# Kernel tuning notes

Measured on AMD Instinct MI355X. Metric: run time of the kernel, lower is better.

## Reference

```python
import jax, jax.numpy as jnp
import numpy as np

EPS = 0.1
MAX_ITER = 100
THRESH = 0.1


def setup_inputs() -> dict:
    key = jax.random.key(0)
    k1, k2, k3, k4 = jax.random.split(key, 4)
    N, P1, P2, D = 4, 1024, 1024, 16
    x = jax.random.normal(k1, (N, P1, D), dtype=jnp.float32)
    y = jax.random.normal(k2, (N, P2, D), dtype=jnp.float32)
    wx = jax.random.uniform(k3, (N, P1), dtype=jnp.float32)
    wy = jax.random.uniform(k4, (N, P2), dtype=jnp.float32)
    # normalize to probability weights (typical usage for empirical measures)
    wx = wx / jnp.sum(wx, axis=-1, keepdims=True)
    wy = wy / jnp.sum(wy, axis=-1, keepdims=True)
    return {"x": x, "y": y, "wx": wx, "wy": wy}


def _cost_matrix(x, y):
    # |x_i - y_j|^1 summed over feature dim -> [N, P1, P2]
    return jnp.sum(jnp.abs(x[:, :, None, :] - y[:, None, :, :]), axis=-1)


def reference(x, y, wx, wy):
    C = _cost_matrix(x, y)                     # [N, P1, P2]
    mu, nu = wx, wy                            # [N, P1], [N, P2]
    log_mu = jnp.log(mu + 1e-8)
    log_nu = jnp.log(nu + 1e-8)

    def M(u, v):
        # (-C_ij + u_i + v_j) / eps
        return (-C + u[:, :, None] + v[:, None, :]) / EPS

    def step(carry, _):
        u, v, done = carry
        u_new = EPS * (log_mu - jax.nn.logsumexp(M(u, v), axis=-1)) + u
        v_new = EPS * (log_nu - jax.nn.logsumexp(M(u_new, v), axis=-2)) + v
        err = jnp.mean(jnp.sum(jnp.abs(u_new - u), axis=-1))
        # emulate torch's early break: freeze u,v once converged
        u_out = jnp.where(done, u, u_new)
        v_out = jnp.where(done, v, v_new)
        done = done | (err < THRESH)
        return (u_out, v_out, done), None

    u0 = jnp.zeros_like(mu)
    v0 = jnp.zeros_like(nu)
    (u, v, _), _ = jax.lax.scan(step, (u0, v0, jnp.array(False)), None, length=MAX_ITER)

    pi = jnp.exp(M(u, v))                      # transport plan [N, P1, P2]
    cost = jnp.sum(pi * C, axis=(-2, -1))      # [N]  (reduction='none')
    return cost, pi, C
```

## Files before the change

### kernel.cpp

```cpp
#include <hip/hip_runtime.h>

static constexpr int   NB      = 4;
static constexpr int   PP      = 1024;
static constexpr int   DD      = 16;
static constexpr float EPSV    = 0.1f;
static constexpr float KE      = 14.42695041f;
static constexpr float KL      = 0.0693147181f;
static constexpr int   MAXIT   = 100;
static constexpr float THRESHV = 0.1f;

static constexpr int NBLK = 256;
static constexpr int NTHR = 512;
static constexpr unsigned DONEG = 1000000u;

static constexpr int    ERR_F_OFF     = 4352;
static constexpr size_t WS_ZERO_BYTES = 4352 * 4;
static constexpr size_t ERR_BYTES     = 512 * 4;

static constexpr int VSNAP_OFF = 131072;

__device__ __forceinline__ float fexp2(float v) { return __builtin_amdgcn_exp2f(v); }
__device__ __forceinline__ float flog2(float v) { return __builtin_amdgcn_logf(v); }

__device__ __forceinline__ float aload(const float* p) {
    return __hip_atomic_load(p, __ATOMIC_RELAXED, __HIP_MEMORY_SCOPE_AGENT);
}
__device__ __forceinline__ void astore(float* p, float v) {
    __hip_atomic_store(p, v, __ATOMIC_RELAXED, __HIP_MEMORY_SCOPE_AGENT);
}
__device__ __forceinline__ unsigned aloadu(const unsigned* p) {
    return __hip_atomic_load(p, __ATOMIC_RELAXED, __HIP_MEMORY_SCOPE_AGENT);
}
__device__ __forceinline__ void astoreu(unsigned* p, unsigned v) {
    __hip_atomic_store(p, v, __ATOMIC_RELAXED, __HIP_MEMORY_SCOPE_AGENT);
}
__device__ __forceinline__ float2 aload2(const float* p) {
    unsigned long long v = __hip_atomic_load((const unsigned long long*)p,
                                             __ATOMIC_RELAXED, __HIP_MEMORY_SCOPE_AGENT);
    union { unsigned long long u; float f[2]; } c; c.u = v;
    return make_float2(c.f[0], c.f[1]);
}
__device__ __forceinline__ void astore2(float* p, float a, float b) {
    union { unsigned long long u; float f[2]; } c; c.f[0] = a; c.f[1] = b;
    __hip_atomic_store((unsigned long long*)p, c.u,
                       __ATOMIC_RELAXED, __HIP_MEMORY_SCOPE_AGENT);
}

__device__ __forceinline__ int pidx(int e) { return (e >> 4) * 17 + (e & 15); }

__device__ __forceinline__ void stage_poll(const unsigned* ws32, int n,
                                           const float* src, unsigned gen,
                                           float* sbuf2, int tid) {
    if (tid < 64) {
        const unsigned* sp = ws32 + (n * 64 + tid) * 16;
        const float* cp = src + tid * 16;
        float2 d0, d1, d2, d3, d4, d5, d6, d7;
        bool got = false;
        for (;;) {
            if (!got && aloadu(sp) >= gen) {
                d0 = aload2(cp + 0);  d1 = aload2(cp + 2);
                d2 = aload2(cp + 4);  d3 = aload2(cp + 6);
                d4 = aload2(cp + 8);  d5 = aload2(cp + 10);
                d6 = aload2(cp + 12); d7 = aload2(cp + 14);
                got = true;
            }
            if (__ballot(got) == ~0ull) break;
            __builtin_amdgcn_s_sleep(1);
        }
        float* dst = sbuf2 + tid * 17;
        dst[0]  = d0.x; dst[1]  = d0.y; dst[2]  = d1.x; dst[3]  = d1.y;
        dst[4]  = d2.x; dst[5]  = d2.y; dst[6]  = d3.x; dst[7]  = d3.y;
        dst[8]  = d4.x; dst[9]  = d4.y; dst[10] = d5.x; dst[11] = d5.y;
        dst[12] = d6.x; dst[13] = d6.y; dst[14] = d7.x; dst[15] = d7.y;
    }
}

__device__ __forceinline__ void gbar_group(unsigned* ws32, int n, int g, unsigned gen) {
    __syncthreads();
    if (threadIdx.x < 64) {
        if (threadIdx.x == 0) astoreu(ws32 + (n * 64 + g) * 16, gen);
        const unsigned* sp = ws32 + (n * 64 + threadIdx.x) * 16;
        while (__ballot(aloadu(sp) >= gen) != ~0ull)
            __builtin_amdgcn_s_sleep(1);
    }
    __syncthreads();
}

__global__ __launch_bounds__(NTHR, 2)
void sinkhorn_kernel(const float* __restrict__ x, const float* __restrict__ y,
                     const float* __restrict__ wx, const float* __restrict__ wy,
                     float* __restrict__ out, float* __restrict__ ws)
{
    __shared__ float rt[16 * PP];
    __shared__ float sbuf2[1088];
    __shared__ float cred[8];
    __shared__ int   Ts;
    __shared__ int   s_ef;

    unsigned* ws32  = (unsigned*)ws;
    unsigned* Tslot = ws32 + 4096;
    unsigned* exitf = ws32 + 4104;
    float*    ews   = ws + ERR_F_OFF;

    float* out_cost = out;
    float* out_pi   = out + NB;
    float* out_C    = out + NB + (size_t)NB * PP * PP;

    const int b   = blockIdx.x;
    const int n   = b >> 6;
    const int g   = b & 63;
    const int i0  = g * 16;
    const int w   = threadIdx.x >> 6;
    const int l   = threadIdx.x & 63;
    const int tid = threadIdx.x;

    float* sc = out_C + (size_t)n * PP * PP;

    if (tid == 0) s_ef = 0;

    float4 xr[2][4];
    #pragma unroll
    for (int rr = 0; rr < 2; ++rr) {
        const float4* xp = (const float4*)(x + ((size_t)n * PP + (i0 + 2 * w + rr)) * DD);
        #pragma unroll
        for (int q = 0; q < 4; ++q) xr[rr][q] = xp[q];
    }
    #pragma unroll 4
    for (int k = 0; k < 16; ++k) {
        int j = l + 64 * k;
        const float4* yp = (const float4*)(y + ((size_t)n * PP + j) * DD);
        float4 y0 = yp[0], y1 = yp[1], y2 = yp[2], y3 = yp[3];
        #pragma unroll
        for (int rr = 0; rr < 2; ++rr) {
            float c = fabsf(xr[rr][0].x - y0.x) + fabsf(xr[rr][0].y - y0.y)
                    + fabsf(xr[rr][0].z - y0.z) + fabsf(xr[rr][0].w - y0.w)
                    + fabsf(xr[rr][1].x - y1.x) + fabsf(xr[rr][1].y - y1.y)
                    + fabsf(xr[rr][1].z - y1.z) + fabsf(xr[rr][1].w - y1.w)
                    + fabsf(xr[rr][2].x - y2.x) + fabsf(xr[rr][2].y - y2.y)
                    + fabsf(xr[rr][2].z - y2.z) + fabsf(xr[rr][2].w - y2.w)
                    + fabsf(xr[rr][3].x - y3.x) + fabsf(xr[rr][3].y - y3.y)
                    + fabsf(xr[rr][3].z - y3.z) + fabsf(xr[rr][3].w - y3.w);
            rt[(2 * w + rr) * PP + j] = c;
        }
    }

    float4 yc[2][4];
    #pragma unroll
    for (int c = 0; c < 2; ++c) {
        const float4* yp = (const float4*)(y + ((size_t)n * PP + (i0 + 2 * w + c)) * DD);
        #pragma unroll
        for (int q = 0; q < 4; ++q) yc[c][q] = yp[q];
    }
    float2 c2[16];
    #pragma unroll 4
    for (int k = 0; k < 16; ++k) {
        const float4* xp = (const float4*)(x + ((size_t)n * PP + (l + 64 * k)) * DD);
        float4 x0 = xp[0], x1 = xp[1], x2 = xp[2], x3 = xp[3];
        float cc[2];
        #pragma unroll
        for (int c = 0; c < 2; ++c) {
            cc[c] = fabsf(x0.x - yc[c][0].x) + fabsf(x0.y - yc[c][0].y)
                  + fabsf(x0.z - yc[c][0].z) + fabsf(x0.w - yc[c][0].w)
                  + fabsf(x1.x - yc[c][1].x) + fabsf(x1.y - yc[c][1].y)
                  + fabsf(x1.z - yc[c][1].z) + fabsf(x1.w - yc[c][1].w)
                  + fabsf(x2.x - yc[c][2].x) + fabsf(x2.y - yc[c][2].y)
                  + fabsf(x2.z - yc[c][2].z) + fabsf(x2.w - yc[c][2].w)
                  + fabsf(x3.x - yc[c][3].x) + fabsf(x3.y - yc[c][3].y)
                  + fabsf(x3.z - yc[c][3].z) + fabsf(x3.w - yc[c][3].w);
        }
        c2[k] = make_float2(cc[0], cc[1]);
    }

    float lmu[2], lnu[2];
    #pragma unroll
    for (int rr = 0; rr < 2; ++rr) {
        lmu[rr] = __logf(wx[n * PP + i0 + 2 * w + rr] + 1e-8f);
        lnu[rr] = __logf(wy[n * PP + i0 + 2 * w + rr] + 1e-8f);
    }

    float uprev0 = 0.f, uprev1 = 0.f;

    int last_t = 0;

    #pragma unroll 1
    for (int t = 0; t < MAXIT; ++t) {
        if (t >= 2 && s_ef != 0 && t >= s_ef + 1) break;
        last_t = t;

        if (t == 0) {
            sbuf2[pidx(2 * tid)] = 0.f; sbuf2[pidx(2 * tid + 1)] = 0.f;
        } else {
            stage_poll(ws32, n, sc + VSNAP_OFF + (size_t)(t - 1) * PP,
                       (unsigned)(2 * t), sbuf2, tid);
        }
        __syncthreads();

        {
            float4 tt[2][4];
            float m0 = -3.4e38f, m1 = -3.4e38f;
            #pragma unroll
            for (int k = 0; k < 4; ++k) {
                int j = 256 * k + 4 * l;
                float v0 = sbuf2[pidx(j)],     v1 = sbuf2[pidx(j + 1)];
                float v2 = sbuf2[pidx(j + 2)], v3 = sbuf2[pidx(j + 3)];
                float4 ca = *(const float4*)&rt[(2 * w) * PP + j];
                float4 cb = *(const float4*)&rt[(2 * w + 1) * PP + j];
                tt[0][k] = make_float4(v0 - ca.x, v1 - ca.y, v2 - ca.z, v3 - ca.w);
                tt[1][k] = make_float4(v0 - cb.x, v1 - cb.y, v2 - cb.z, v3 - cb.w);
                m0 = fmaxf(m0, fmaxf(fmaxf(tt[0][k].x, tt[0][k].y), fmaxf(tt[0][k].z, tt[0][k].w)));
                m1 = fmaxf(m1, fmaxf(fmaxf(tt[1][k].x, tt[1][k].y), fmaxf(tt[1][k].z, tt[1][k].w)));
            }
            #pragma unroll
            for (int off = 32; off >= 1; off >>= 1) {
                m0 = fmaxf(m0, __shfl_xor(m0, off));
                m1 = fmaxf(m1, __shfl_xor(m1, off));
            }
            float s0 = 0.f, s1 = 0.f;
            #pragma unroll
            for (int k = 0; k < 4; ++k) {
                s0 += fexp2((tt[0][k].x - m0) * KE) + fexp2((tt[0][k].y - m0) * KE)
                    + fexp2((tt[0][k].z - m0) * KE) + fexp2((tt[0][k].w - m0) * KE);
                s1 += fexp2((tt[1][k].x - m1) * KE) + fexp2((tt[1][k].y - m1) * KE)
                    + fexp2((tt[1][k].z - m1) * KE) + fexp2((tt[1][k].w - m1) * KE);
            }
            #pragma unroll
            for (int off = 32; off >= 1; off >>= 1) {
                s0 += __shfl_xor(s0, off);
                s1 += __shfl_xor(s1, off);
            }
            float un0 = EPSV * lmu[0] - (m0 + KL * flog2(s0));
            float un1 = EPSV * lmu[1] - (m1 + KL * flog2(s1));
            if (l == 0) astore2(sc + (size_t)t * PP + i0 + 2 * w, un0, un1);
        }
        __syncthreads();
        if (tid == 0) astoreu(ws32 + (n * 64 + g) * 16, (unsigned)(2 * t + 1));

        stage_poll(ws32, n, sc + (size_t)t * PP, (unsigned)(2 * t + 1), sbuf2, tid);
        __syncthreads();

        {
            float up0 = sbuf2[pidx(2 * tid)], up1 = sbuf2[pidx(2 * tid + 1)];
            float we = fabsf(up0 - uprev0) + fabsf(up1 - uprev1);
            uprev0 = up0; uprev1 = up1;
            #pragma unroll
            for (int off = 32; off >= 1; off >>= 1) we += __shfl_xor(we, off);
            if (l == 0) cred[w] = we;
        }
        __syncthreads();

        {
            float tt0[16], tt1[16], m0 = -3.4e38f, m1 = -3.4e38f;
            #pragma unroll
            for (int k = 0; k < 16; ++k) {
                float uu = sbuf2[pidx(l + 64 * k)];
                tt0[k] = uu - c2[k].x;
                tt1[k] = uu - c2[k].y;
                m0 = fmaxf(m0, tt0[k]);
                m1 = fmaxf(m1, tt1[k]);
            }
            #pragma unroll
            for (int off = 32; off >= 1; off >>= 1) {
                m0 = fmaxf(m0, __shfl_xor(m0, off));
                m1 = fmaxf(m1, __shfl_xor(m1, off));
            }
            float s0 = 0.f, s1 = 0.f;
            #pragma unroll
            for (int k = 0; k < 16; ++k) {
                s0 += fexp2((tt0[k] - m0) * KE);
                s1 += fexp2((tt1[k] - m1) * KE);
            }
            #pragma unroll
            for (int off = 32; off >= 1; off >>= 1) {
                s0 += __shfl_xor(s0, off);
                s1 += __shfl_xor(s1, off);
            }
            float vn0 = EPSV * lnu[0] - (m0 + KL * flog2(s0));
            float vn1 = EPSV * lnu[1] - (m1 + KL * flog2(s1));
            if (l == 0)
                astore2(sc + VSNAP_OFF + (size_t)t * PP + i0 + 2 * w, vn0, vn1);
        }
        if (g == 0 && tid == 0) {
            float es = cred[0] + cred[1] + cred[2] + cred[3]
                     + cred[4] + cred[5] + cred[6] + cred[7];
            astore(ews + n * 128 + t, es);
        }

        __syncthreads();
        if (tid < 64) {
            if (tid == 0) astoreu(ws32 + (n * 64 + g) * 16, (unsigned)(2 * t + 2));
            if (g == 0) {
                float s1f = aload(ews + 0 * 128 + tid) + aload(ews + 1 * 128 + tid)
                          + aload(ews + 2 * 128 + tid) + aload(ews + 3 * 128 + tid);
                float s2f = aload(ews + 0 * 128 + 64 + tid) + aload(ews + 1 * 128 + 64 + tid)
                          + aload(ews + 2 * 128 + 64 + tid) + aload(ews + 3 * 128 + 64 + tid);
                unsigned long long bb = __ballot(s1f < THRESHV * (float)NB)
                                      | __ballot(s2f < THRESHV * (float)NB);
                if (bb != 0ull && tid == 0 && aloadu(exitf + n) == 0u)
                    astoreu(exitf + n, (unsigned)(t + 1));
            }
        }
        if (tid == 0) s_ef = (int)aloadu(exitf + n);
        __syncthreads();
    }

    {
        const unsigned need = (unsigned)(2 * last_t + 2);
        if (tid < 64) {
            const unsigned* sp = ws32 + (n * 64 + tid) * 16;
            while (__ballot(aloadu(sp) >= need) != ~0ull)
                __builtin_amdgcn_s_sleep(1);
        }
        __syncthreads();
    }

    if (g == 0 && tid == 0) astoreu(ws32 + (n * 64) * 16, DONEG);

    if (b == 0 && tid < 64) {
        for (;;) {
            bool ok = (tid >= 4) || (aloadu(ws32 + tid * 64 * 16) >= DONEG);
            if (__ballot(ok) == ~0ull) break;
            __builtin_amdgcn_s_sleep(2);
        }
        float s1f = aload(ews + 0 * 128 + tid) + aload(ews + 1 * 128 + tid)
                  + aload(ews + 2 * 128 + tid) + aload(ews + 3 * 128 + tid);
        float s2f = aload(ews + 0 * 128 + 64 + tid) + aload(ews + 1 * 128 + 64 + tid)
                  + aload(ews + 2 * 128 + 64 + tid) + aload(ews + 3 * 128 + 64 + tid);
        unsigned long long b1 = __ballot(s1f < THRESHV * (float)NB);
        unsigned long long b2 = __ballot(s2f < THRESHV * (float)NB);
        int T = b1 ? (__ffsll((long long)b1) - 1)
                   : (b2 ? 64 + (__ffsll((long long)b2) - 1) : MAXIT - 1);
        if (tid == 0) astoreu(Tslot, (unsigned)(T + 1));
    }
    if (tid == 0) {
        unsigned tv;
        while ((tv = aloadu(Tslot)) == 0u) __builtin_amdgcn_s_sleep(2);
        Ts = (int)tv - 1;
    }
    __syncthreads();
    const int T = Ts;

    float u_loc[2];
    {
        float2 up = aload2(sc + (size_t)T * PP + i0 + 2 * w);
        u_loc[0] = up.x; u_loc[1] = up.y;
        float2 vp = aload2(sc + VSNAP_OFF + (size_t)T * PP + 2 * tid);
        sbuf2[pidx(2 * tid)] = vp.x; sbuf2[pidx(2 * tid + 1)] = vp.y;
    }
    gbar_group(ws32, n, g, DONEG + 1u);

    float cacc = 0.f;
    #pragma unroll
    for (int rr = 0; rr < 2; ++rr) {
        int r = 2 * w + rr;
        int i = i0 + r;
        float un = u_loc[rr];
        #pragma unroll
        for (int k = 0; k < 4; ++k) {
            int j = 256 * k + 4 * l;
            float4 c4 = *(const float4*)&rt[r * PP + j];
            float v0 = sbuf2[pidx(j)],     v1 = sbuf2[pidx(j + 1)];
            float v2 = sbuf2[pidx(j + 2)], v3 = sbuf2[pidx(j + 3)];
            float4 p4;
            p4.x = fexp2((un + v0 - c4.x) * KE);
            p4.y = fexp2((un + v1 - c4.y) * KE);
            p4.z = fexp2((un + v2 - c4.z) * KE);
            p4.w = fexp2((un + v3 - c4.w) * KE);
            *(float4*)&out_pi[((size_t)n * PP + i) * PP + j] = p4;
            *(float4*)&out_C [((size_t)n * PP + i) * PP + j] = c4;
            cacc += p4.x * c4.x + p4.y * c4.y + p4.z * c4.z + p4.w * c4.w;
        }
    }
    #pragma unroll
    for (int off = 32; off >= 1; off >>= 1) cacc += __shfl_xor(cacc, off);
    if (l == 0) cred[w] = cacc;
    __syncthreads();
    if (tid == 0) {
        float s = 0.f;
        #pragma unroll
        for (int q = 0; q < 8; ++q) s += cred[q];
        atomicAdd(&out_cost[n], s);
    }
}

extern "C" void kernel_launch(void* const* d_in, const int* in_sizes, int n_in,
                              void* d_out, int out_size, void* d_ws, size_t ws_size,
                              hipStream_t stream) {
    const float* x  = (const float*)d_in[0];
    const float* y  = (const float*)d_in[1];
    const float* wx = (const float*)d_in[2];
    const float* wy = (const float*)d_in[3];
    float* out = (float*)d_out;
    float* ws  = (float*)d_ws;

    (void)hipMemsetAsync(d_ws, 0, WS_ZERO_BYTES, stream);
    (void)hipMemsetAsync((char*)d_ws + WS_ZERO_BYTES, 0x7f, ERR_BYTES, stream);
    (void)hipMemsetAsync(d_out, 0, NB * sizeof(float), stream);

    hipLaunchKernelGGL(sinkhorn_kernel, dim3(NBLK), dim3(NTHR), 0, stream,
                       x, y, wx, wy, out, ws);
}
```

Baseline: 797.1 us.

## Halve block count with 1024-thread blocks of 32 rows and XOR-swizzled LDS buffer

Each block now owns 32 rows with 1024 threads, so only 32 groups per batch take part in the per-iteration cross-block flag barrier instead of 64. The intent is to cut polling and synchronisation latency in each Sinkhorn half-step. The padded shared buffer (pidx) is replaced by an XOR-swizzled layout so u/v can be read as float4 without bank conflicts. The price is a larger LDS footprint (32 rows of cost per block) and more complex index mapping, with a risk of layout errors in the many hard-coded index paths.

```diff
diff --git a/kernel.cpp b/kernel.cpp
--- a/kernel.cpp
+++ b/kernel.cpp
@@ -9,8 +9,10 @@
 static constexpr int   MAXIT   = 100;
 static constexpr float THRESHV = 0.1f;
 
-static constexpr int NBLK = 256;
-static constexpr int NTHR = 512;
+static constexpr int NBLK = 128;
+static constexpr int NTHR = 1024;
+static constexpr int GPB  = 32;
+static constexpr int RPB  = 32;
 static constexpr unsigned DONEG = 1000000u;
 
 static constexpr int    ERR_F_OFF     = 4352;
@@ -46,54 +48,55 @@
                        __ATOMIC_RELAXED, __HIP_MEMORY_SCOPE_AGENT);
 }
 
-__device__ __forceinline__ int pidx(int e) { return (e >> 4) * 17 + (e & 15); }
 
 __device__ __forceinline__ void stage_poll(const unsigned* ws32, int n,
                                            const float* src, unsigned gen,
-                                           float* sbuf2, int tid) {
+                                           float* sbuf, int tid) {
     if (tid < 64) {
-        const unsigned* sp = ws32 + (n * 64 + tid) * 16;
-        const float* cp = src + tid * 16;
-        float2 d0, d1, d2, d3, d4, d5, d6, d7;
-        bool got = false;
+        const int t = tid & 31;
+        bool got = (tid >= 32);
+        const unsigned* sp = ws32 + (n * GPB + t) * 16;
+        const float* cp = src + t * RPB;
+        float2 d[16];
         for (;;) {
             if (!got && aloadu(sp) >= gen) {
-                d0 = aload2(cp + 0);  d1 = aload2(cp + 2);
-                d2 = aload2(cp + 4);  d3 = aload2(cp + 6);
-                d4 = aload2(cp + 8);  d5 = aload2(cp + 10);
-                d6 = aload2(cp + 12); d7 = aload2(cp + 14);
+                #pragma unroll
+                for (int q = 0; q < 16; ++q) d[q] = aload2(cp + 2 * q);
                 got = true;
             }
             if (__ballot(got) == ~0ull) break;
             __builtin_amdgcn_s_sleep(1);
         }
-        float* dst = sbuf2 + tid * 17;
-        dst[0]  = d0.x; dst[1]  = d0.y; dst[2]  = d1.x; dst[3]  = d1.y;
-        dst[4]  = d2.x; dst[5]  = d2.y; dst[6]  = d3.x; dst[7]  = d3.y;
-        dst[8]  = d4.x; dst[9]  = d4.y; dst[10] = d5.x; dst[11] = d5.y;
-        dst[12] = d6.x; dst[13] = d6.y; dst[14] = d7.x; dst[15] = d7.y;
+        if (tid < 32) {
+            #pragma unroll
+            for (int q = 0; q < 8; ++q) {
+                int p = (8 * t + q) ^ (t & 7);
+                *(float4*)&sbuf[4 * p] =
+                    make_float4(d[2 * q].x, d[2 * q].y, d[2 * q + 1].x, d[2 * q + 1].y);
+            }
+        }
     }
 }
 
 __device__ __forceinline__ void gbar_group(unsigned* ws32, int n, int g, unsigned gen) {
     __syncthreads();
     if (threadIdx.x < 64) {
-        if (threadIdx.x == 0) astoreu(ws32 + (n * 64 + g) * 16, gen);
-        const unsigned* sp = ws32 + (n * 64 + threadIdx.x) * 16;
-        while (__ballot(aloadu(sp) >= gen) != ~0ull)
+        if (threadIdx.x == 0) astoreu(ws32 + (n * GPB + g) * 16, gen);
+        const unsigned* sp = ws32 + (n * GPB + (threadIdx.x & 31)) * 16;
+        while (__ballot((threadIdx.x >= 32) || (aloadu(sp) >= gen)) != ~0ull)
             __builtin_amdgcn_s_sleep(1);
     }
     __syncthreads();
 }
 
-__global__ __launch_bounds__(NTHR, 2)
+__global__ __launch_bounds__(NTHR, 4)
 void sinkhorn_kernel(const float* __restrict__ x, const float* __restrict__ y,
                      const float* __restrict__ wx, const float* __restrict__ wy,
                      float* __restrict__ out, float* __restrict__ ws)
 {
-    __shared__ float rt[16 * PP];
-    __shared__ float sbuf2[1088];
-    __shared__ float cred[8];
+    __shared__ float rt[RPB * PP];
+    __shared__ float sbuf[PP];
+    __shared__ float cred[16];
     __shared__ int   Ts;
     __shared__ int   s_ef;
 
@@ -107,9 +110,9 @@
     float* out_C    = out + NB + (size_t)NB * PP * PP;
 
     const int b   = blockIdx.x;
-    const int n   = b >> 6;
-    const int g   = b & 63;
-    const int i0  = g * 16;
+    const int n   = b >> 5;
+    const int g   = b & (GPB - 1);
+    const int i0  = g * RPB;
     const int w   = threadIdx.x >> 6;
     const int l   = threadIdx.x & 63;
     const int tid = threadIdx.x;
@@ -117,6 +120,21 @@
     float* sc = out_C + (size_t)n * PP * PP;
 
     if (tid == 0) s_ef = 0;
+
+    const int lx = l ^ ((l >> 3) & 7);
+    int rv[16];
+    #pragma unroll
+    for (int k = 0; k < 16; ++k) {
+        int s = 16 * k + (l >> 2);
+        int p = s ^ ((2 * k + (l >> 5)) & 7);
+        rv[k] = 4 * p + (l & 3);
+    }
+    int ea;
+    {
+        int s = tid >> 1;
+        int p = s ^ ((tid >> 4) & 7);
+        ea = 4 * p + 2 * (tid & 1);
+    }
 
     float4 xr[2][4];
     #pragma unroll
@@ -188,10 +206,10 @@
         last_t = t;
 
         if (t == 0) {
-            sbuf2[pidx(2 * tid)] = 0.f; sbuf2[pidx(2 * tid + 1)] = 0.f;
+            if (tid < 512) { sbuf[ea] = 0.f; sbuf[ea + 1] = 0.f; }
         } else {
             stage_poll(ws32, n, sc + VSNAP_OFF + (size_t)(t - 1) * PP,
-                       (unsigned)(2 * t), sbuf2, tid);
+                       (unsigned)(2 * t), sbuf, tid);
         }
         __syncthreads();
 
@@ -201,12 +219,11 @@
             #pragma unroll
             for (int k = 0; k < 4; ++k) {
                 int j = 256 * k + 4 * l;
-                float v0 = sbuf2[pidx(j)],     v1 = sbuf2[pidx(j + 1)];
-                float v2 = sbuf2[pidx(j + 2)], v3 = sbuf2[pidx(j + 3)];
+                float4 v4 = *(const float4*)&sbuf[256 * k + 4 * lx];
                 float4 ca = *(const float4*)&rt[(2 * w) * PP + j];
                 float4 cb = *(const float4*)&rt[(2 * w + 1) * PP + j];
-                tt[0][k] = make_float4(v0 - ca.x, v1 - ca.y, v2 - ca.z, v3 - ca.w);
-                tt[1][k] = make_float4(v0 - cb.x, v1 - cb.y, v2 - cb.z, v3 - cb.w);
+                tt[0][k] = make_float4(v4.x - ca.x, v4.y - ca.y, v4.z - ca.z, v4.w - ca.w);
+                tt[1][k] = make_float4(v4.x - cb.x, v4.y - cb.y, v4.z - cb.z, v4.w - cb.w);
                 m0 = fmaxf(m0, fmaxf(fmaxf(tt[0][k].x, tt[0][k].y), fmaxf(tt[0][k].z, tt[0][k].w)));
                 m1 = fmaxf(m1, fmaxf(fmaxf(tt[1][k].x, tt[1][k].y), fmaxf(tt[1][k].z, tt[1][k].w)));
             }
@@ -233,13 +250,13 @@
             if (l == 0) astore2(sc + (size_t)t * PP + i0 + 2 * w, un0, un1);
         }
         __syncthreads();
-        if (tid == 0) astoreu(ws32 + (n * 64 + g) * 16, (unsigned)(2 * t + 1));
-
-        stage_poll(ws32, n, sc + (size_t)t * PP, (unsigned)(2 * t + 1), sbuf2, tid);
-        __syncthreads();
-
-        {
-            float up0 = sbuf2[pidx(2 * tid)], up1 = sbuf2[pidx(2 * tid + 1)];
+        if (tid == 0) astoreu(ws32 + (n * GPB + g) * 16, (unsigned)(2 * t + 1));
+
+        stage_poll(ws32, n, sc + (size_t)t * PP, (unsigned)(2 * t + 1), sbuf, tid);
+        __syncthreads();
+
+        if (tid < 512) {
+            float up0 = sbuf[ea], up1 = sbuf[ea + 1];
             float we = fabsf(up0 - uprev0) + fabsf(up1 - uprev1);
             uprev0 = up0; uprev1 = up1;
             #pragma unroll
@@ -252,7 +269,7 @@
             float tt0[16], tt1[16], m0 = -3.4e38f, m1 = -3.4e38f;
             #pragma unroll
             for (int k = 0; k < 16; ++k) {
-                float uu = sbuf2[pidx(l + 64 * k)];
+                float uu = sbuf[rv[k]];
                 tt0[k] = uu - c2[k].x;
                 tt1[k] = uu - c2[k].y;
                 m0 = fmaxf(m0, tt0[k]);
@@ -287,7 +304,7 @@
 
         __syncthreads();
         if (tid < 64) {
-            if (tid == 0) astoreu(ws32 + (n * 64 + g) * 16, (unsigned)(2 * t + 2));
+            if (tid == 0) astoreu(ws32 + (n * GPB + g) * 16, (unsigned)(2 * t + 2));
             if (g == 0) {
                 float s1f = aload(ews + 0 * 128 + tid) + aload(ews + 1 * 128 + tid)
                           + aload(ews + 2 * 128 + tid) + aload(ews + 3 * 128 + tid);
@@ -306,18 +323,18 @@
     {
         const unsigned need = (unsigned)(2 * last_t + 2);
         if (tid < 64) {
-            const unsigned* sp = ws32 + (n * 64 + tid) * 16;
-            while (__ballot(aloadu(sp) >= need) != ~0ull)
+            const unsigned* sp = ws32 + (n * GPB + (tid & 31)) * 16;
+            while (__ballot((tid >= 32) || (aloadu(sp) >= need)) != ~0ull)
                 __builtin_amdgcn_s_sleep(1);
         }
         __syncthreads();
     }
 
-    if (g == 0 && tid == 0) astoreu(ws32 + (n * 64) * 16, DONEG);
+    if (g == 0 && tid == 0) astoreu(ws32 + (n * GPB) * 16, DONEG);
 
     if (b == 0 && tid < 64) {
         for (;;) {
-            bool ok = (tid >= 4) || (aloadu(ws32 + tid * 64 * 16) >= DONEG);
+            bool ok = (tid >= 4) || (aloadu(ws32 + tid * GPB * 16) >= DONEG);
             if (__ballot(ok) == ~0ull) break;
             __builtin_amdgcn_s_sleep(2);
         }
@@ -343,8 +360,10 @@
     {
         float2 up = aload2(sc + (size_t)T * PP + i0 + 2 * w);
         u_loc[0] = up.x; u_loc[1] = up.y;
-        float2 vp = aload2(sc + VSNAP_OFF + (size_t)T * PP + 2 * tid);
-        sbuf2[pidx(2 * tid)] = vp.x; sbuf2[pidx(2 * tid + 1)] = vp.y;
+        if (tid < 512) {
+            float2 vp = aload2(sc + VSNAP_OFF + (size_t)T * PP + 2 * tid);
+            sbuf[ea] = vp.x; sbuf[ea + 1] = vp.y;
+        }
     }
     gbar_group(ws32, n, g, DONEG + 1u);
 
@@ -358,13 +377,12 @@
         for (int k = 0; k < 4; ++k) {
             int j = 256 * k + 4 * l;
             float4 c4 = *(const float4*)&rt[r * PP + j];
-            float v0 = sbuf2[pidx(j)],     v1 = sbuf2[pidx(j + 1)];
-            float v2 = sbuf2[pidx(j + 2)], v3 = sbuf2[pidx(j + 3)];
+            float4 v4 = *(const float4*)&sbuf[256 * k + 4 * lx];
             float4 p4;
-            p4.x = fexp2((un + v0 - c4.x) * KE);
-            p4.y = fexp2((un + v1 - c4.y) * KE);
-            p4.z = fexp2((un + v2 - c4.z) * KE);
-            p4.w = fexp2((un + v3 - c4.w) * KE);
+            p4.x = fexp2((un + v4.x - c4.x) * KE);
+            p4.y = fexp2((un + v4.y - c4.y) * KE);
+            p4.z = fexp2((un + v4.z - c4.z) * KE);
+            p4.w = fexp2((un + v4.w - c4.w) * KE);
             *(float4*)&out_pi[((size_t)n * PP + i) * PP + j] = p4;
             *(float4*)&out_C [((size_t)n * PP + i) * PP + j] = c4;
             cacc += p4.x * c4.x + p4.y * c4.y + p4.z * c4.z + p4.w * c4.w;
@@ -377,7 +395,7 @@
     if (tid == 0) {
         float s = 0.f;
         #pragma unroll
-        for (int q = 0; q < 8; ++q) s += cred[q];
+        for (int q = 0; q < 16; ++q) s += cred[q];
         atomicAdd(&out_cost[n], s);
     }
 }
```

Result: slower. 1.098 ms (+37.7%).

## Swizzle shared vector buffer for float4 access and shorten convergence-detect critical path

Applied to the files above, without the earlier changes.

Replaces the padded (17-stride) shared staging buffer with an XOR-swizzled dense layout so staged u/v vectors are written and read as float4, cutting LDS instruction count and bank conflicts. It also removes a __syncthreads by prefetching the error history loads early and folding the local error into the detect step, and adds a per-block flag so detection stops once it has fired. The snapshot region is shifted by a small offset. The risks are subtle index mismatches in the swizzle and changed ordering between the error store and the detection read.

```diff
diff --git a/kernel.cpp b/kernel.cpp
--- a/kernel.cpp
+++ b/kernel.cpp
@@ -17,7 +17,8 @@
 static constexpr size_t WS_ZERO_BYTES = 4352 * 4;
 static constexpr size_t ERR_BYTES     = 512 * 4;
 
-static constexpr int VSNAP_OFF = 131072;
+static constexpr int SNAP_SHIFT = 12;
+static constexpr int VSNAP_OFF  = 131072;
 
 __device__ __forceinline__ float fexp2(float v) { return __builtin_amdgcn_exp2f(v); }
 __device__ __forceinline__ float flog2(float v) { return __builtin_amdgcn_logf(v); }
@@ -46,11 +47,10 @@
                        __ATOMIC_RELAXED, __HIP_MEMORY_SCOPE_AGENT);
 }
 
-__device__ __forceinline__ int pidx(int e) { return (e >> 4) * 17 + (e & 15); }
 
 __device__ __forceinline__ void stage_poll(const unsigned* ws32, int n,
                                            const float* src, unsigned gen,
-                                           float* sbuf2, int tid) {
+                                           float* sbuf, int tid) {
     if (tid < 64) {
         const unsigned* sp = ws32 + (n * 64 + tid) * 16;
         const float* cp = src + tid * 16;
@@ -67,11 +67,11 @@
             if (__ballot(got) == ~0ull) break;
             __builtin_amdgcn_s_sleep(1);
         }
-        float* dst = sbuf2 + tid * 17;
-        dst[0]  = d0.x; dst[1]  = d0.y; dst[2]  = d1.x; dst[3]  = d1.y;
-        dst[4]  = d2.x; dst[5]  = d2.y; dst[6]  = d3.x; dst[7]  = d3.y;
-        dst[8]  = d4.x; dst[9]  = d4.y; dst[10] = d5.x; dst[11] = d5.y;
-        dst[12] = d6.x; dst[13] = d6.y; dst[14] = d7.x; dst[15] = d7.y;
+        const int m = (tid >> 1) & 7;
+        *(float4*)&sbuf[4 * ((4 * tid + 0) ^ m)] = make_float4(d0.x, d0.y, d1.x, d1.y);
+        *(float4*)&sbuf[4 * ((4 * tid + 1) ^ m)] = make_float4(d2.x, d2.y, d3.x, d3.y);
+        *(float4*)&sbuf[4 * ((4 * tid + 2) ^ m)] = make_float4(d4.x, d4.y, d5.x, d5.y);
+        *(float4*)&sbuf[4 * ((4 * tid + 3) ^ m)] = make_float4(d6.x, d6.y, d7.x, d7.y);
     }
 }
 
@@ -92,10 +92,11 @@
                      float* __restrict__ out, float* __restrict__ ws)
 {
     __shared__ float rt[16 * PP];
-    __shared__ float sbuf2[1088];
+    __shared__ float sbuf[PP];
     __shared__ float cred[8];
     __shared__ int   Ts;
     __shared__ int   s_ef;
+    __shared__ int   s_fired;
 
     unsigned* ws32  = (unsigned*)ws;
     unsigned* Tslot = ws32 + 4096;
@@ -114,9 +115,22 @@
     const int l   = threadIdx.x & 63;
     const int tid = threadIdx.x;
 
-    float* sc = out_C + (size_t)n * PP * PP;
-
-    if (tid == 0) s_ef = 0;
+    float* sc = out_C + (size_t)n * PP * PP + SNAP_SHIFT;
+
+    if (tid == 0) { s_ef = 0; s_fired = 0; }
+
+    const int lx = l ^ ((l >> 3) & 7);
+    int rv[16];
+    #pragma unroll
+    for (int k = 0; k < 16; ++k) {
+        int s = 16 * k + (l >> 2);
+        rv[k] = 4 * (s ^ ((2 * k + (l >> 5)) & 7)) + (l & 3);
+    }
+    int ea;
+    {
+        int s = tid >> 1;
+        ea = 4 * (s ^ ((tid >> 4) & 7)) + 2 * (tid & 1);
+    }
 
     float4 xr[2][4];
     #pragma unroll
@@ -188,10 +202,10 @@
         last_t = t;
 
         if (t == 0) {
-            sbuf2[pidx(2 * tid)] = 0.f; sbuf2[pidx(2 * tid + 1)] = 0.f;
+            sbuf[ea] = 0.f; sbuf[ea + 1] = 0.f;
         } else {
             stage_poll(ws32, n, sc + VSNAP_OFF + (size_t)(t - 1) * PP,
-                       (unsigned)(2 * t), sbuf2, tid);
+                       (unsigned)(2 * t), sbuf, tid);
         }
         __syncthreads();
 
@@ -201,12 +215,11 @@
             #pragma unroll
             for (int k = 0; k < 4; ++k) {
                 int j = 256 * k + 4 * l;
-                float v0 = sbuf2[pidx(j)],     v1 = sbuf2[pidx(j + 1)];
-                float v2 = sbuf2[pidx(j + 2)], v3 = sbuf2[pidx(j + 3)];
+                float4 v4 = *(const float4*)&sbuf[256 * k + 4 * lx];
                 float4 ca = *(const float4*)&rt[(2 * w) * PP + j];
                 float4 cb = *(const float4*)&rt[(2 * w + 1) * PP + j];
-                tt[0][k] = make_float4(v0 - ca.x, v1 - ca.y, v2 - ca.z, v3 - ca.w);
-                tt[1][k] = make_float4(v0 - cb.x, v1 - cb.y, v2 - cb.z, v3 - cb.w);
+                tt[0][k] = make_float4(v4.x - ca.x, v4.y - ca.y, v4.z - ca.z, v4.w - ca.w);
+                tt[1][k] = make_float4(v4.x - cb.x, v4.y - cb.y, v4.z - cb.z, v4.w - cb.w);
                 m0 = fmaxf(m0, fmaxf(fmaxf(tt[0][k].x, tt[0][k].y), fmaxf(tt[0][k].z, tt[0][k].w)));
                 m1 = fmaxf(m1, fmaxf(fmaxf(tt[1][k].x, tt[1][k].y), fmaxf(tt[1][k].z, tt[1][k].w)));
             }
@@ -235,24 +248,33 @@
         __syncthreads();
         if (tid == 0) astoreu(ws32 + (n * 64 + g) * 16, (unsigned)(2 * t + 1));
 
-        stage_poll(ws32, n, sc + (size_t)t * PP, (unsigned)(2 * t + 1), sbuf2, tid);
+        stage_poll(ws32, n, sc + (size_t)t * PP, (unsigned)(2 * t + 1), sbuf, tid);
         __syncthreads();
 
         {
-            float up0 = sbuf2[pidx(2 * tid)], up1 = sbuf2[pidx(2 * tid + 1)];
+            float up0 = sbuf[ea], up1 = sbuf[ea + 1];
             float we = fabsf(up0 - uprev0) + fabsf(up1 - uprev1);
             uprev0 = up0; uprev1 = up1;
             #pragma unroll
             for (int off = 32; off >= 1; off >>= 1) we += __shfl_xor(we, off);
             if (l == 0) cred[w] = we;
         }
-        __syncthreads();
+
+        float dl1[4], dl2[4];
+        const bool do_det = (g == 0) && (tid < 64) && (s_fired == 0);
+        if (do_det) {
+            #pragma unroll
+            for (int q = 0; q < NB; ++q) {
+                dl1[q] = aload(ews + q * 128 + tid);
+                dl2[q] = aload(ews + q * 128 + 64 + tid);
+            }
+        }
 
         {
             float tt0[16], tt1[16], m0 = -3.4e38f, m1 = -3.4e38f;
             #pragma unroll
             for (int k = 0; k < 16; ++k) {
-                float uu = sbuf2[pidx(l + 64 * k)];
+                float uu = sbuf[rv[k]];
                 tt0[k] = uu - c2[k].x;
                 tt1[k] = uu - c2[k].y;
                 m0 = fmaxf(m0, tt0[k]);
@@ -279,24 +301,32 @@
             if (l == 0)
                 astore2(sc + VSNAP_OFF + (size_t)t * PP + i0 + 2 * w, vn0, vn1);
         }
-        if (g == 0 && tid == 0) {
-            float es = cred[0] + cred[1] + cred[2] + cred[3]
-                     + cred[4] + cred[5] + cred[6] + cred[7];
-            astore(ews + n * 128 + t, es);
-        }
 
         __syncthreads();
         if (tid < 64) {
             if (tid == 0) astoreu(ws32 + (n * 64 + g) * 16, (unsigned)(2 * t + 2));
             if (g == 0) {
-                float s1f = aload(ews + 0 * 128 + tid) + aload(ews + 1 * 128 + tid)
-                          + aload(ews + 2 * 128 + tid) + aload(ews + 3 * 128 + tid);
-                float s2f = aload(ews + 0 * 128 + 64 + tid) + aload(ews + 1 * 128 + 64 + tid)
-                          + aload(ews + 2 * 128 + 64 + tid) + aload(ews + 3 * 128 + 64 + tid);
-                unsigned long long bb = __ballot(s1f < THRESHV * (float)NB)
-                                      | __ballot(s2f < THRESHV * (float)NB);
-                if (bb != 0ull && tid == 0 && aloadu(exitf + n) == 0u)
-                    astoreu(exitf + n, (unsigned)(t + 1));
+                float esl = cred[0] + cred[1] + cred[2] + cred[3]
+                          + cred[4] + cred[5] + cred[6] + cred[7];
+                if (tid == 0) astore(ews + n * 128 + t, esl);
+                if (s_fired == 0) {
+                    float s1f = 0.f, s2f = 0.f;
+                    #pragma unroll
+                    for (int q = 0; q < NB; ++q) {
+                        float e1 = dl1[q], e2 = dl2[q];
+                        if (q == n) {
+                            if (tid == t)      e1 = esl;
+                            if (64 + tid == t) e2 = esl;
+                        }
+                        s1f += e1; s2f += e2;
+                    }
+                    unsigned long long bb = __ballot(s1f < THRESHV * (float)NB)
+                                          | __ballot(s2f < THRESHV * (float)NB);
+                    if (tid == 0 && bb != 0ull) {
+                        astoreu(exitf + n, (unsigned)(t + 1));
+                        s_fired = 1;
+                    }
+                }
             }
         }
         if (tid == 0) s_ef = (int)aloadu(exitf + n);
@@ -344,7 +374,7 @@
         float2 up = aload2(sc + (size_t)T * PP + i0 + 2 * w);
         u_loc[0] = up.x; u_loc[1] = up.y;
         float2 vp = aload2(sc + VSNAP_OFF + (size_t)T * PP + 2 * tid);
-        sbuf2[pidx(2 * tid)] = vp.x; sbuf2[pidx(2 * tid + 1)] = vp.y;
+        sbuf[ea] = vp.x; sbuf[ea + 1] = vp.y;
     }
     gbar_group(ws32, n, g, DONEG + 1u);
 
@@ -358,13 +388,12 @@
         for (int k = 0; k < 4; ++k) {
             int j = 256 * k + 4 * l;
             float4 c4 = *(const float4*)&rt[r * PP + j];
-            float v0 = sbuf2[pidx(j)],     v1 = sbuf2[pidx(j + 1)];
-            float v2 = sbuf2[pidx(j + 2)], v3 = sbuf2[pidx(j + 3)];
+            float4 v4 = *(const float4*)&sbuf[256 * k + 4 * lx];
             float4 p4;
-            p4.x = fexp2((un + v0 - c4.x) * KE);
-            p4.y = fexp2((un + v1 - c4.y) * KE);
-            p4.z = fexp2((un + v2 - c4.z) * KE);
-            p4.w = fexp2((un + v3 - c4.w) * KE);
+            p4.x = fexp2((un + v4.x - c4.x) * KE);
+            p4.y = fexp2((un + v4.y - c4.y) * KE);
+            p4.z = fexp2((un + v4.z - c4.z) * KE);
+            p4.w = fexp2((un + v4.w - c4.w) * KE);
             *(float4*)&out_pi[((size_t)n * PP + i) * PP + j] = p4;
             *(float4*)&out_C [((size_t)n * PP + i) * PP + j] = c4;
             cacc += p4.x * c4.x + p4.y * c4.y + p4.z * c4.z + p4.w * c4.w;
```

New measurement: 880.0 us. +10.4%, slower.
